# Performance work log

Measured on AMD Instinct MI355X. Metric: run time of the kernel, lower is better.

The kernel has to match this reference:

```python
import jax, jax.numpy as jnp
import numpy as np
from jax import lax

EPS = 1e-5
NBIT = 127.0  # 8-bit symmetric: 2^(8-1)-1

def ste_round(x):
    return x + lax.stop_gradient(jnp.round(x) - x)

def quant_act(x, rng_max):
    # symmetric fake-quant of activations with learned per-cluster range
    s = rng_max / NBIT
    xq = jnp.clip(ste_round(x / s), -NBIT, NBIT) * s
    return xq, s

def fold_bn(w, gamma, beta, mean, var):
    std = jnp.sqrt(var + EPS)
    scale = gamma / std
    w_f = w * scale[:, None, None, None]
    b_f = beta - mean * scale
    return w_f, b_f

def quant_weight(w):
    # per-output-channel symmetric quant
    s = jnp.max(jnp.abs(w), axis=(1, 2, 3), keepdims=True) / NBIT
    wq = jnp.clip(ste_round(w / s), -NBIT, NBIT) * s
    return wq, s.reshape(-1)

def conv(x, w, stride=1, groups=1, pad=0):
    return lax.conv_general_dilated(
        x, w, window_strides=(stride, stride),
        padding=((pad, pad), (pad, pad)),
        dimension_numbers=('NCHW', 'OIHW', 'NCHW'),
        feature_group_count=groups)

def setup_inputs() -> dict:
    key = jax.random.key(0)
    ks = jax.random.split(key, 24)
    B, Cin, H, W = 64, 96, 28, 28
    Cmid, Cout, NC = 576, 96, 4
    d = {}
    d['x'] = jax.random.normal(ks[0], (B, Cin, H, W), dtype=jnp.float32)
    # conv1: 1x1 expansion
    d['w1'] = jax.random.normal(ks[1], (Cmid, Cin, 1, 1), jnp.float32) * 0.1
    d['g1'] = jax.random.uniform(ks[2], (Cmid,), minval=0.5, maxval=1.5)
    d['b1'] = jax.random.normal(ks[3], (Cmid,)) * 0.1
    d['m1'] = jax.random.normal(ks[4], (Cmid,)) * 0.1
    d['v1'] = jax.random.uniform(ks[5], (Cmid,), minval=0.5, maxval=1.5)
    # conv2: 3x3 depthwise
    d['w2'] = jax.random.normal(ks[6], (Cmid, 1, 3, 3), jnp.float32) * 0.1
    d['g2'] = jax.random.uniform(ks[7], (Cmid,), minval=0.5, maxval=1.5)
    d['b2'] = jax.random.normal(ks[8], (Cmid,)) * 0.1
    d['m2'] = jax.random.normal(ks[9], (Cmid,)) * 0.1
    d['v2'] = jax.random.uniform(ks[10], (Cmid,), minval=0.5, maxval=1.5)
    # conv3: 1x1 projection
    d['w3'] = jax.random.normal(ks[11], (Cout, Cmid, 1, 1), jnp.float32) * 0.1
    d['g3'] = jax.random.uniform(ks[12], (Cout,), minval=0.5, maxval=1.5)
    d['b3'] = jax.random.normal(ks[13], (Cout,)) * 0.1
    d['m3'] = jax.random.normal(ks[14], (Cout,)) * 0.1
    d['v3'] = jax.random.uniform(ks[15], (Cout,), minval=0.5, maxval=1.5)
    # per-cluster learned activation ranges for the 4 QuantAct modules
    d['r0'] = jax.random.uniform(ks[16], (NC,), minval=2.0, maxval=8.0)
    d['r1'] = jax.random.uniform(ks[17], (NC,), minval=2.0, maxval=8.0)
    d['r2'] = jax.random.uniform(ks[18], (NC,), minval=2.0, maxval=8.0)
    d['r3'] = jax.random.uniform(ks[19], (NC,), minval=2.0, maxval=8.0)
    d['cluster'] = 2
    return d

def reference(x, w1, g1, b1, m1, v1, w2, g2, b2, m2, v2,
              w3, g3, b3, m3, v3, r0, r1, r2, r3, cluster):
    identity = x  # residual path (in==out, stride==1)
    # QuantAct -> conv1 (BN-folded, per-channel quant) -> ReLU6
    xq, s0 = quant_act(x, r0[cluster])
    w1f, bf1 = fold_bn(w1, g1, b1, m1, v1)
    w1q, ws1 = quant_weight(w1f)
    y = conv(xq, w1q) + bf1[None, :, None, None]
    y = jnp.clip(y, 0.0, 6.0)
    # QuantAct1 -> depthwise conv2 -> ReLU6
    yq, s1 = quant_act(y, r1[cluster])
    w2f, bf2 = fold_bn(w2, g2, b2, m2, v2)
    w2q, ws2 = quant_weight(w2f)
    y = conv(yq, w2q, stride=1, groups=w2.shape[0], pad=1) + bf2[None, :, None, None]
    y = jnp.clip(y, 0.0, 6.0)
    # QuantAct2 -> conv3 projection
    yq, s2 = quant_act(y, r2[cluster])
    w3f, bf3 = fold_bn(w3, g3, b3, m3, v3)
    w3q, ws3 = quant_weight(w3f)
    y = conv(yq, w3q) + bf3[None, :, None, None]
    # residual add, then int32 requant
    y = y + identity
    out, s3 = quant_act(y, r3[cluster])
    return out, s3
```

## Files before the change

kernel.cpp:

```cpp
#include <hip/hip_runtime.h>
#include <cstdint>
#include <cstddef>

typedef int   v4i __attribute__((ext_vector_type(4)));
typedef float v4f __attribute__((ext_vector_type(4)));
typedef unsigned int u32;

constexpr int B_   = 64;
constexpr int CIN  = 96;
constexpr int P_   = 784;
constexpr int CMID = 576;
constexpr int COUT = 96;
constexpr int NOUT = B_ * COUT * P_;
constexpr float NBITF = 127.0f;
constexpr float EPSF  = 1e-5f;


__device__ __forceinline__ int dot3(u32 win, u32 wpk, int acc) {
#if __has_builtin(__builtin_amdgcn_sdot4)
    return __builtin_amdgcn_sdot4((int)win, (int)wpk, acc, false);
#else
    return acc + (int)(signed char)(win)        * (int)(signed char)(wpk)
               + (int)(signed char)(win >> 8)   * (int)(signed char)(wpk >> 8)
               + (int)(signed char)(win >> 16)  * (int)(signed char)(wpk >> 16);
#endif
}

__global__ __launch_bounds__(64)
void prep_weights(const float* __restrict__ w1, const float* __restrict__ g1,
                  const float* __restrict__ b1, const float* __restrict__ m1,
                  const float* __restrict__ v1,
                  const float* __restrict__ w2, const float* __restrict__ g2,
                  const float* __restrict__ b2, const float* __restrict__ m2,
                  const float* __restrict__ v2,
                  const float* __restrict__ w3, const float* __restrict__ g3,
                  const float* __restrict__ b3, const float* __restrict__ m3,
                  const float* __restrict__ v3,
                  int8_t* __restrict__ w1qp, float* __restrict__ ws1, float* __restrict__ bf1,
                  int8_t* __restrict__ w2qi, float* __restrict__ ws2, float* __restrict__ bf2,
                  int8_t* __restrict__ w3qp, float* __restrict__ ws3, float* __restrict__ bf3)
{
    int blk  = blockIdx.x;
    int lane = threadIdx.x;

    const float *w, *g, *bb, *mm, *vv;
    int oc, K, which;
    if (blk < CMID)            { which = 0; w = w1; g = g1; bb = b1; mm = m1; vv = v1; oc = blk;            K = CIN;  }
    else if (blk < 2 * CMID)   { which = 1; w = w2; g = g2; bb = b2; mm = m2; vv = v2; oc = blk - CMID;     K = 9;    }
    else                       { which = 2; w = w3; g = g3; bb = b3; mm = m3; vv = v3; oc = blk - 2 * CMID; K = CMID; }

    float scale = g[oc] / sqrtf(vv[oc] + EPSF);

    float mx = 0.f;
    for (int k = lane; k < K; k += 64)
        mx = fmaxf(mx, fabsf(w[oc * K + k] * scale));
    #pragma unroll
    for (int off = 1; off < 64; off <<= 1)
        mx = fmaxf(mx, __shfl_xor(mx, off));

    float s = mx / NBITF;

    for (int k = lane; k < K; k += 64) {
        float wf = w[oc * K + k] * scale;
        float q  = fminf(fmaxf(rintf(wf / s), -127.f), 127.f);
        if (which == 0)      w1qp[oc * 144 + k] = (int8_t)q;
        else if (which == 1) w2qi[oc * 12 + k]  = (int8_t)q;
        else                 w3qp[oc * 592 + k] = (int8_t)q;
    }
    if (which == 0 && lane < 12)
        ((u32*)(w1qp + oc * 144))[24 + lane] = 0u;
    if (lane == 0) {
        float bf = bb[oc] - mm[oc] * scale;
        if (which == 0)      { ws1[oc] = s; bf1[oc] = bf; }
        else if (which == 1) { ws2[oc] = s; bf2[oc] = bf; }
        else                 { ws3[oc] = s; bf3[oc] = bf; }
    }
}

__global__ __launch_bounds__(256)
void quant_x(const float* __restrict__ x, const float* __restrict__ r0,
             const int* __restrict__ cluster, int8_t* __restrict__ x8t)
{
    __shared__ u32 T[112 * 37];

    int tid = threadIdx.x, pt = blockIdx.x, b = blockIdx.y;
    float inv_s0 = NBITF / r0[cluster[0]];

    for (int i = tid; i < 112 * 13; i += 256) {
        int row = i / 13, cpad = i - row * 13;
        T[row * 37 + 24 + cpad] = 0u;
    }
    for (int u = tid; u < 24 * 28; u += 256) {
        int pq = u % 28, icq = u / 28;
        int pxb = pt * 112 + pq * 4;
        int q[4][4];
        #pragma unroll
        for (int j = 0; j < 4; j++) {
            v4f xv = *(const v4f*)(x + ((size_t)b * CIN + icq * 4 + j) * P_ + pxb);
            #pragma unroll
            for (int i = 0; i < 4; i++)
                q[j][i] = (int)fminf(fmaxf(rintf(xv[i] * inv_s0), -127.f), 127.f);
        }
        #pragma unroll
        for (int i = 0; i < 4; i++) {
            u32 t0 = __builtin_amdgcn_perm((u32)q[1][i], (u32)q[0][i], 0x00000400u);
            u32 t1 = __builtin_amdgcn_perm((u32)q[3][i], (u32)q[2][i], 0x00000400u);
            T[(pq * 4 + i) * 37 + icq] = __builtin_amdgcn_perm(t1, t0, 0x05040100u);
        }
    }
    __syncthreads();
    u32* gdst = (u32*)x8t;
    for (int i = tid; i < 112 * 36; i += 256) {
        int row = i / 36, cc = i - row * 36;
        gdst[((size_t)b * P_ + pt * 112 + row) * 36 + cc] = T[row * 37 + cc];
    }
}

__global__ __launch_bounds__(256)
void conv12(const int8_t* __restrict__ x8t, const int8_t* __restrict__ w1qp,
            const float* __restrict__ ws1, const float* __restrict__ bf1,
            const int8_t* __restrict__ w2qi, const float* __restrict__ ws2,
            const float* __restrict__ bf2,
            const float* __restrict__ r0, const float* __restrict__ r1,
            const float* __restrict__ r2, const int* __restrict__ cluster,
            int8_t* __restrict__ y2qT)
{
    __shared__ int8_t AY[192 * 144];
    __shared__ int8_t y1s[192 * 132];

    int tid = threadIdx.x;
    int b   = blockIdx.y;
    int mt  = blockIdx.x / 14, rt = blockIdx.x - mt * 14;
    int oc0 = mt * 192;
    int R0  = rt * 2;
    int W0  = (R0 - 1) * 28;

    int   c      = cluster[0];
    float s0     = r0[c] / NBITF;
    float s1     = r1[c] / NBITF;
    float inv_s1 = NBITF / r1[c];
    float inv_s2 = NBITF / r2[c];
    float u1     = fminf(rintf(6.f * inv_s1), 127.f);
    float u2     = fminf(rintf(6.f * inv_s2), 127.f);

    {
        const v4i* gsrc = (const v4i*)(w1qp + (size_t)oc0 * 144);
        v4i* ldst = (v4i*)AY;
        for (int i = tid; i < 192 * 9; i += 256) ldst[i] = gsrc[i];
    }
    __syncthreads();

    int lane = tid & 63, wv = tid >> 6;
    int n = lane & 15, q4 = lane >> 4;

    const v4i* bp[7];
    #pragma unroll
    for (int j = 0; j < 7; j++) {
        int px = W0 + j * 16 + n;
        px = min(max(px, 0), P_ - 1);
        bp[j] = (const v4i*)(x8t + ((size_t)b * P_ + px) * 144) + q4;
    }

    v4i acc[3][7];
    #pragma unroll
    for (int i = 0; i < 3; i++)
        #pragma unroll
        for (int j = 0; j < 7; j++) acc[i][j] = (v4i){0, 0, 0, 0};

    const v4i* Af = (const v4i*)AY;
    #pragma unroll
    for (int ks = 0; ks < 2; ks++) {
        v4i bfr[7], afr[3];
        #pragma unroll
        for (int j = 0; j < 7; j++) bfr[j] = bp[j][ks * 4];
        #pragma unroll
        for (int i = 0; i < 3; i++)
            afr[i] = Af[(wv * 48 + i * 16 + n) * 9 + ks * 4 + q4];
        #pragma unroll
        for (int i = 0; i < 3; i++)
            #pragma unroll
            for (int j = 0; j < 7; j++)
                acc[i][j] = __builtin_amdgcn_mfma_i32_16x16x64_i8(afr[i], bfr[j], acc[i][j], 0, 0, 0);
    }

    float sA[3][4], bA[3][4];
    #pragma unroll
    for (int i = 0; i < 3; i++)
        #pragma unroll
        for (int r = 0; r < 4; r++) {
            int oc = oc0 + wv * 48 + i * 16 + q4 * 4 + r;
            sA[i][r] = s0 * ws1[oc] * inv_s1;
            bA[i][r] = bf1[oc] * inv_s1;
        }
    for (int i = tid; i < 192 * 4; i += 256) {
        int ch = i >> 2, r = i & 3;
        int8_t* p = y1s + ch * 132 + r * 32;
        p[0] = 0; p[29] = 0; *(short*)(p + 30) = 0;
    }
    #pragma unroll
    for (int i = 0; i < 3; i++)
        #pragma unroll
        for (int j = 0; j < 7; j++) {
            int pxl = j * 16 + n;
            bool valid = (unsigned)(W0 + pxl) < (unsigned)P_;
            int rowl = pxl / 28, col = pxl - rowl * 28;
            int chl = wv * 48 + i * 16 + q4 * 4;
            #pragma unroll
            for (int r = 0; r < 4; r++) {
                float t = fmaf((float)acc[i][j][r], sA[i][r], bA[i][r]);
                t = fminf(fmaxf(rintf(t), 0.f), u1);
                int lvl = valid ? (int)t : 0;
                y1s[(chl + r) * 132 + rowl * 32 + 1 + col] = (int8_t)lvl;
            }
        }
    __syncthreads();

    int8_t* y2s = AY;
    for (int idx = tid; idx < 192 * 14; idx += 256) {
        int xq   = idx % 7;
        int t2   = idx / 7;
        int orow = t2 & 1;
        int chl  = t2 >> 1;
        int chg  = oc0 + chl;

        const u32* wd = (const u32*)(w2qi + chg * 12);
        u32 wr0 = wd[0], wr1 = wd[1], wr2 = wd[2];
        u32 pk0 = wr0 & 0x00ffffffu;
        u32 pk1 = __builtin_amdgcn_perm(wr1, wr0, 0x00050403u) & 0x00ffffffu;
        u32 pk2 = __builtin_amdgcn_perm(wr2, wr1, 0x00040302u) & 0x00ffffffu;

        const int8_t* base = y1s + chl * 132 + orow * 32;
        int a0 = 0, a1 = 0, a2 = 0, a3 = 0;
        #pragma unroll
        for (int dr = 0; dr < 3; dr++) {
            const u32* row = (const u32*)(base + dr * 32);
            u32 d0 = row[xq], d1 = row[xq + 1];
            u32 pk = (dr == 0) ? pk0 : (dr == 1) ? pk1 : pk2;
            a0 = dot3(d0, pk, a0);
            a1 = dot3(__builtin_amdgcn_alignbyte(d1, d0, 1), pk, a1);
            a2 = dot3(__builtin_amdgcn_alignbyte(d1, d0, 2), pk, a2);
            a3 = dot3(__builtin_amdgcn_alignbyte(d1, d0, 3), pk, a3);
        }
        float sc = s1 * ws2[chg] * inv_s2;
        float bb = bf2[chg] * inv_s2;
        int pxo = orow * 28 + xq * 4;
        int aa[4] = {a0, a1, a2, a3};
        #pragma unroll
        for (int i = 0; i < 4; i++) {
            float t = fmaf((float)aa[i], sc, bb);
            t = fminf(fmaxf(rintf(t), 0.f), u2);
            y2s[(pxo + i) * 200 + chl] = (int8_t)(int)t;
        }
    }
    __syncthreads();

    for (int i = tid; i < 56 * 48; i += 256) {
        int px = i / 48, cq = i - px * 48;
        u32 v = ((const u32*)(y2s + px * 200))[cq];
        ((u32*)y2qT)[((size_t)b * P_ + R0 * 28 + px) * 148 + (oc0 >> 2) + cq] = v;
    }
}

__global__ __launch_bounds__(256)
void conv3_kernel(const int8_t* __restrict__ y2qT, const int8_t* __restrict__ w3qp,
                  const float* __restrict__ ws3, const float* __restrict__ bf3,
                  const float* __restrict__ x, const float* __restrict__ r2,
                  const float* __restrict__ r3, const int* __restrict__ cluster,
                  float* __restrict__ out)
{
    __shared__ int8_t Ash[96 * 592];

    int tid = threadIdx.x, b = blockIdx.y;
    int p0 = blockIdx.x * 64;

    int   c      = cluster[0];
    float s2     = r2[c] / NBITF;
    float s3     = r3[c] / NBITF;
    float inv_s3 = NBITF / r3[c];

    {
        const v4i* gs = (const v4i*)w3qp;
        v4i* ld = (v4i*)Ash;
        for (int i = tid; i < 96 * 37; i += 256) ld[i] = gs[i];
    }
    __syncthreads();

    int lane = tid & 63, wv = tid >> 6;
    int n = lane & 15, q4 = lane >> 4;
    int px  = p0 + wv * 16 + n;
    int pxc = min(px, P_ - 1);

    const v4i* brow = (const v4i*)(y2qT + ((size_t)b * P_ + pxc) * 592) + q4;
    const v4i* Af   = (const v4i*)Ash;

    v4i acc[6];
    #pragma unroll
    for (int i = 0; i < 6; i++) acc[i] = (v4i){0, 0, 0, 0};

    #pragma unroll
    for (int ks = 0; ks < 9; ks++) {
        v4i bfr = brow[ks * 4];
        #pragma unroll
        for (int i = 0; i < 6; i++) {
            v4i afr = Af[(i * 16 + n) * 37 + ks * 4 + q4];
            acc[i] = __builtin_amdgcn_mfma_i32_16x16x64_i8(afr, bfr, acc[i], 0, 0, 0);
        }
    }

    if (px < P_) {
        #pragma unroll
        for (int i = 0; i < 6; i++)
            #pragma unroll
            for (int r = 0; r < 4; r++) {
                int oc = i * 16 + q4 * 4 + r;
                size_t gi = ((size_t)b * COUT + oc) * P_ + px;
                float v  = (float)acc[i][r] * (s2 * ws3[oc]) + bf3[oc] + x[gi];
                float qv = fminf(fmaxf(rintf(v * inv_s3), -127.f), 127.f);
                out[gi] = qv * s3;
            }
    }
    if (blockIdx.x == 0 && blockIdx.y == 0 && tid == 0)
        out[NOUT] = s3;
}

extern "C" void kernel_launch(void* const* d_in, const int* in_sizes, int n_in,
                              void* d_out, int out_size, void* d_ws, size_t ws_size,
                              hipStream_t stream)
{
    const float* x  = (const float*)d_in[0];
    const float* w1 = (const float*)d_in[1];
    const float* g1 = (const float*)d_in[2];
    const float* b1 = (const float*)d_in[3];
    const float* m1 = (const float*)d_in[4];
    const float* v1 = (const float*)d_in[5];
    const float* w2 = (const float*)d_in[6];
    const float* g2 = (const float*)d_in[7];
    const float* b2 = (const float*)d_in[8];
    const float* m2 = (const float*)d_in[9];
    const float* v2 = (const float*)d_in[10];
    const float* w3 = (const float*)d_in[11];
    const float* g3 = (const float*)d_in[12];
    const float* b3 = (const float*)d_in[13];
    const float* m3 = (const float*)d_in[14];
    const float* v3 = (const float*)d_in[15];
    const float* r0 = (const float*)d_in[16];
    const float* r1 = (const float*)d_in[17];
    const float* r2 = (const float*)d_in[18];
    const float* r3 = (const float*)d_in[19];
    const int*   cl = (const int*)d_in[20];

    float* out = (float*)d_out;

    char*  ws  = (char*)d_ws;
    size_t off = 0;
    auto carve = [&](size_t bytes) {
        size_t cur = off;
        off = (off + bytes + 255) & ~(size_t)255;
        return (void*)(ws + cur);
    };
    int8_t* w1qp = (int8_t*)carve((size_t)CMID * 144);
    float*  ws1  = (float*)carve(CMID * 4);
    float*  bf1  = (float*)carve(CMID * 4);
    int8_t* w2qi = (int8_t*)carve((size_t)CMID * 12);
    float*  ws2  = (float*)carve(CMID * 4);
    float*  bf2  = (float*)carve(CMID * 4);
    int8_t* w3qp = (int8_t*)carve((size_t)COUT * 592);
    float*  ws3  = (float*)carve(COUT * 4);
    float*  bf3  = (float*)carve(COUT * 4);
    int8_t* x8t  = (int8_t*)carve((size_t)B_ * P_ * 144);
    int8_t* y2qT = (int8_t*)carve((size_t)B_ * P_ * 592);
    (void)ws_size; (void)in_sizes; (void)n_in; (void)out_size;

    prep_weights<<<dim3(2 * CMID + COUT), dim3(64), 0, stream>>>(
        w1, g1, b1, m1, v1, w2, g2, b2, m2, v2, w3, g3, b3, m3, v3,
        w1qp, ws1, bf1, w2qi, ws2, bf2, w3qp, ws3, bf3);

    quant_x<<<dim3(7, B_), dim3(256), 0, stream>>>(x, r0, cl, x8t);

    conv12<<<dim3(42, B_), dim3(256), 0, stream>>>(
        x8t, w1qp, ws1, bf1, w2qi, ws2, bf2, r0, r1, r2, cl, y2qT);

    conv3_kernel<<<dim3(13, B_), dim3(256), 0, stream>>>(
        y2qT, w3qp, ws3, bf3, x, r2, r3, cl, out);
}
```

Before: 192.3 us.

## Retile int8 intermediates into K-major 64-pixel blocks with packed register transposes

Changes the global layout of the quantized input and the depthwise output from pixel-major rows (144/592 bytes per pixel) to 64-pixel tiles where each 4-channel dword group is contiguous across pixels. MFMA B-fragment loads in conv12 and conv3 become four coalesced dword loads instead of one strided 16-byte load per lane. The shared-memory staging between the 1x1 and depthwise stages is rewritten to pack four channels per dword and transpose with byte-permute instructions instead of doing scattered byte stores. Depthwise weights are also prepacked into 16-byte vectors. The cost is more load instructions per fragment and extra permute work.

```diff
diff --git a/kernel.cpp b/kernel.cpp
--- a/kernel.cpp
+++ b/kernel.cpp
@@ -15,15 +15,30 @@
 constexpr float NBITF = 127.0f;
 constexpr float EPSF  = 1e-5f;
 
-
-__device__ __forceinline__ int dot3(u32 win, u32 wpk, int acc) {
+constexpr int XKD = 36;
+constexpr int YKD = 144;
+constexpr int XBD = 13 * XKD * 64;
+constexpr int YBD = 13 * YKD * 64;
+
+__device__ __forceinline__ int dot3(u32 a, u32 w, int acc) {
 #if __has_builtin(__builtin_amdgcn_sdot4)
-    return __builtin_amdgcn_sdot4((int)win, (int)wpk, acc, false);
+    return __builtin_amdgcn_sdot4((int)a, (int)w, acc, false);
 #else
-    return acc + (int)(signed char)(win)        * (int)(signed char)(wpk)
-               + (int)(signed char)(win >> 8)   * (int)(signed char)(wpk >> 8)
-               + (int)(signed char)(win >> 16)  * (int)(signed char)(wpk >> 16);
+    return acc + (int)(signed char)(a)        * (int)(signed char)(w)
+               + (int)(signed char)(a >> 8)   * (int)(signed char)(w >> 8)
+               + (int)(signed char)(a >> 16)  * (int)(signed char)(w >> 16);
 #endif
+}
+
+__device__ __forceinline__ void tr4(u32 S0, u32 S1, u32 S2, u32 S3, u32 O[4]) {
+    u32 u01 = __builtin_amdgcn_perm(S1, S0, 0x05010400u);
+    u32 u23 = __builtin_amdgcn_perm(S3, S2, 0x05010400u);
+    u32 v01 = __builtin_amdgcn_perm(S1, S0, 0x07030602u);
+    u32 v23 = __builtin_amdgcn_perm(S3, S2, 0x07030602u);
+    O[0] = __builtin_amdgcn_perm(u23, u01, 0x05040100u);
+    O[1] = __builtin_amdgcn_perm(u23, u01, 0x07060302u);
+    O[2] = __builtin_amdgcn_perm(v23, v01, 0x05040100u);
+    O[3] = __builtin_amdgcn_perm(v23, v01, 0x07060302u);
 }
 
 __global__ __launch_bounds__(64)
@@ -37,7 +52,7 @@
                   const float* __restrict__ b3, const float* __restrict__ m3,
                   const float* __restrict__ v3,
                   int8_t* __restrict__ w1qp, float* __restrict__ ws1, float* __restrict__ bf1,
-                  int8_t* __restrict__ w2qi, float* __restrict__ ws2, float* __restrict__ bf2,
+                  v4i* __restrict__ w2pk, float* __restrict__ ws2, float* __restrict__ bf2,
                   int8_t* __restrict__ w3qp, float* __restrict__ ws3, float* __restrict__ bf3)
 {
     int blk  = blockIdx.x;
@@ -60,15 +75,29 @@
 
     float s = mx / NBITF;
 
+    int myq = 0;
     for (int k = lane; k < K; k += 64) {
         float wf = w[oc * K + k] * scale;
         float q  = fminf(fmaxf(rintf(wf / s), -127.f), 127.f);
         if (which == 0)      w1qp[oc * 144 + k] = (int8_t)q;
-        else if (which == 1) w2qi[oc * 12 + k]  = (int8_t)q;
+        else if (which == 1) myq = (int)q;
         else                 w3qp[oc * 592 + k] = (int8_t)q;
     }
     if (which == 0 && lane < 12)
         ((u32*)(w1qp + oc * 144))[24 + lane] = 0u;
+    if (which == 1) {
+        u32 qq[9];
+        #pragma unroll
+        for (int t = 0; t < 9; t++) qq[t] = (u32)__shfl(myq, t, 64) & 0xffu;
+        if (lane == 0) {
+            v4i pk;
+            pk[0] = (int)(qq[0] | (qq[1] << 8) | (qq[2] << 16));
+            pk[1] = (int)(qq[3] | (qq[4] << 8) | (qq[5] << 16));
+            pk[2] = (int)(qq[6] | (qq[7] << 8) | (qq[8] << 16));
+            pk[3] = 0;
+            w2pk[oc] = pk;
+        }
+    }
     if (lane == 0) {
         float bf = bb[oc] - mm[oc] * scale;
         if (which == 0)      { ws1[oc] = s; bf1[oc] = bf; }
@@ -79,20 +108,20 @@
 
 __global__ __launch_bounds__(256)
 void quant_x(const float* __restrict__ x, const float* __restrict__ r0,
-             const int* __restrict__ cluster, int8_t* __restrict__ x8t)
+             const int* __restrict__ cluster, u32* __restrict__ x8t)
 {
     __shared__ u32 T[112 * 37];
 
-    int tid = threadIdx.x, pt = blockIdx.x, b = blockIdx.y;
+    int tid = threadIdx.x, pt0 = blockIdx.x, b = blockIdx.y;
     float inv_s0 = NBITF / r0[cluster[0]];
 
-    for (int i = tid; i < 112 * 13; i += 256) {
-        int row = i / 13, cpad = i - row * 13;
+    for (int i = tid; i < 112 * 12; i += 256) {
+        int row = i / 12, cpad = i - row * 12;
         T[row * 37 + 24 + cpad] = 0u;
     }
     for (int u = tid; u < 24 * 28; u += 256) {
         int pq = u % 28, icq = u / 28;
-        int pxb = pt * 112 + pq * 4;
+        int pxb = pt0 * 112 + pq * 4;
         int q[4][4];
         #pragma unroll
         for (int j = 0; j < 4; j++) {
@@ -109,24 +138,25 @@
         }
     }
     __syncthreads();
-    u32* gdst = (u32*)x8t;
-    for (int i = tid; i < 112 * 36; i += 256) {
-        int row = i / 36, cc = i - row * 36;
-        gdst[((size_t)b * P_ + pt * 112 + row) * 36 + cc] = T[row * 37 + cc];
+    u32* gb = x8t + (size_t)b * XBD;
+    for (int i = tid; i < XKD * 112; i += 256) {
+        int icq = i / 112, pxo = i - icq * 112;
+        int px = pt0 * 112 + pxo;
+        gb[(((px >> 6) * XKD) + icq) * 64 + (px & 63)] = T[pxo * 37 + icq];
     }
 }
 
 __global__ __launch_bounds__(256)
-void conv12(const int8_t* __restrict__ x8t, const int8_t* __restrict__ w1qp,
+void conv12(const u32* __restrict__ x8t, const int8_t* __restrict__ w1qp,
             const float* __restrict__ ws1, const float* __restrict__ bf1,
-            const int8_t* __restrict__ w2qi, const float* __restrict__ ws2,
+            const v4i* __restrict__ w2pk, const float* __restrict__ ws2,
             const float* __restrict__ bf2,
             const float* __restrict__ r0, const float* __restrict__ r1,
             const float* __restrict__ r2, const int* __restrict__ cluster,
-            int8_t* __restrict__ y2qT)
+            u32* __restrict__ y2qT)
 {
-    __shared__ int8_t AY[192 * 144];
-    __shared__ int8_t y1s[192 * 132];
+    __shared__ u32 AY[6912];
+    __shared__ u32 PB[5488];
 
     int tid = threadIdx.x;
     int b   = blockIdx.y;
@@ -144,21 +174,22 @@
     float u2     = fminf(rintf(6.f * inv_s2), 127.f);
 
     {
-        const v4i* gsrc = (const v4i*)(w1qp + (size_t)oc0 * 144);
-        v4i* ldst = (v4i*)AY;
-        for (int i = tid; i < 192 * 9; i += 256) ldst[i] = gsrc[i];
+        const v4i* gs = (const v4i*)(w1qp + (size_t)oc0 * 144);
+        v4i* ld = (v4i*)AY;
+        for (int i = tid; i < 192 * 9; i += 256) ld[i] = gs[i];
     }
     __syncthreads();
 
     int lane = tid & 63, wv = tid >> 6;
     int n = lane & 15, q4 = lane >> 4;
 
-    const v4i* bp[7];
+    const u32* xb = x8t + (size_t)b * XBD;
+    int pbase[7];
     #pragma unroll
     for (int j = 0; j < 7; j++) {
         int px = W0 + j * 16 + n;
         px = min(max(px, 0), P_ - 1);
-        bp[j] = (const v4i*)(x8t + ((size_t)b * P_ + px) * 144) + q4;
+        pbase[j] = ((px >> 6) * XKD) * 64 + (px & 63);
     }
 
     v4i acc[3][7];
@@ -170,9 +201,16 @@
     const v4i* Af = (const v4i*)AY;
     #pragma unroll
     for (int ks = 0; ks < 2; ks++) {
+        int k0 = ks * 16 + q4 * 4;
         v4i bfr[7], afr[3];
         #pragma unroll
-        for (int j = 0; j < 7; j++) bfr[j] = bp[j][ks * 4];
+        for (int j = 0; j < 7; j++) {
+            u32 d0 = xb[pbase[j] + (k0 + 0) * 64];
+            u32 d1 = xb[pbase[j] + (k0 + 1) * 64];
+            u32 d2 = xb[pbase[j] + (k0 + 2) * 64];
+            u32 d3 = xb[pbase[j] + (k0 + 3) * 64];
+            bfr[j] = (v4i){(int)d0, (int)d1, (int)d2, (int)d3};
+        }
         #pragma unroll
         for (int i = 0; i < 3; i++)
             afr[i] = Af[(wv * 48 + i * 16 + n) * 9 + ks * 4 + q4];
@@ -192,50 +230,56 @@
             sA[i][r] = s0 * ws1[oc] * inv_s1;
             bA[i][r] = bf1[oc] * inv_s1;
         }
-    for (int i = tid; i < 192 * 4; i += 256) {
-        int ch = i >> 2, r = i & 3;
-        int8_t* p = y1s + ch * 132 + r * 32;
-        p[0] = 0; p[29] = 0; *(short*)(p + 30) = 0;
-    }
-    #pragma unroll
-    for (int i = 0; i < 3; i++)
+    #pragma unroll
+    for (int i = 0; i < 3; i++) {
+        int chq = wv * 12 + i * 4 + q4;
         #pragma unroll
         for (int j = 0; j < 7; j++) {
             int pxl = j * 16 + n;
             bool valid = (unsigned)(W0 + pxl) < (unsigned)P_;
-            int rowl = pxl / 28, col = pxl - rowl * 28;
-            int chl = wv * 48 + i * 16 + q4 * 4;
+            u32 pk = 0;
             #pragma unroll
             for (int r = 0; r < 4; r++) {
                 float t = fmaf((float)acc[i][j][r], sA[i][r], bA[i][r]);
                 t = fminf(fmaxf(rintf(t), 0.f), u1);
-                int lvl = valid ? (int)t : 0;
-                y1s[(chl + r) * 132 + rowl * 32 + 1 + col] = (int8_t)lvl;
+                pk |= ((u32)(int)t) << (8 * r);
             }
-        }
-    __syncthreads();
-
-    int8_t* y2s = AY;
-    for (int idx = tid; idx < 192 * 14; idx += 256) {
-        int xq   = idx % 7;
-        int t2   = idx / 7;
+            PB[pxl * 49 + chq] = valid ? pk : 0u;
+        }
+    }
+    __syncthreads();
+
+    for (int u = tid; u < 1536; u += 256) {
+        int cc = u & 7, rowl = (u >> 3) & 3, chq = u >> 5;
+        u32 S[4];
+        #pragma unroll
+        for (int k = 0; k < 4; k++) {
+            int col = 4 * cc - 1 + k;
+            S[k] = ((unsigned)col < 28u) ? PB[(rowl * 28 + col) * 49 + chq] : 0u;
+        }
+        u32 O[4];
+        tr4(S[0], S[1], S[2], S[3], O);
+        int bse = chq * 132 + rowl * 8 + cc;
+        #pragma unroll
+        for (int r = 0; r < 4; r++) AY[bse + r * 33] = O[r];
+    }
+    __syncthreads();
+
+    for (int u = tid; u < 2688; u += 256) {
+        int xq = u % 7;
+        int t2 = u / 7;
         int orow = t2 & 1;
         int chl  = t2 >> 1;
         int chg  = oc0 + chl;
 
-        const u32* wd = (const u32*)(w2qi + chg * 12);
-        u32 wr0 = wd[0], wr1 = wd[1], wr2 = wd[2];
-        u32 pk0 = wr0 & 0x00ffffffu;
-        u32 pk1 = __builtin_amdgcn_perm(wr1, wr0, 0x00050403u) & 0x00ffffffu;
-        u32 pk2 = __builtin_amdgcn_perm(wr2, wr1, 0x00040302u) & 0x00ffffffu;
-
-        const int8_t* base = y1s + chl * 132 + orow * 32;
+        v4i wpk = w2pk[chg];
+        int base = chl * 33 + orow * 8;
         int a0 = 0, a1 = 0, a2 = 0, a3 = 0;
         #pragma unroll
         for (int dr = 0; dr < 3; dr++) {
-            const u32* row = (const u32*)(base + dr * 32);
-            u32 d0 = row[xq], d1 = row[xq + 1];
-            u32 pk = (dr == 0) ? pk0 : (dr == 1) ? pk1 : pk2;
+            u32 d0 = AY[base + dr * 8 + xq];
+            u32 d1 = AY[base + dr * 8 + xq + 1];
+            u32 pk = (u32)((dr == 0) ? wpk[0] : (dr == 1) ? wpk[1] : wpk[2]);
             a0 = dot3(d0, pk, a0);
             a1 = dot3(__builtin_amdgcn_alignbyte(d1, d0, 1), pk, a1);
             a2 = dot3(__builtin_amdgcn_alignbyte(d1, d0, 2), pk, a2);
@@ -243,35 +287,46 @@
         }
         float sc = s1 * ws2[chg] * inv_s2;
         float bb = bf2[chg] * inv_s2;
-        int pxo = orow * 28 + xq * 4;
         int aa[4] = {a0, a1, a2, a3};
+        u32 pk2 = 0;
         #pragma unroll
         for (int i = 0; i < 4; i++) {
             float t = fmaf((float)aa[i], sc, bb);
             t = fminf(fmaxf(rintf(t), 0.f), u2);
-            y2s[(pxo + i) * 200 + chl] = (int8_t)(int)t;
-        }
-    }
-    __syncthreads();
-
-    for (int i = tid; i < 56 * 48; i += 256) {
-        int px = i / 48, cq = i - px * 48;
-        u32 v = ((const u32*)(y2s + px * 200))[cq];
-        ((u32*)y2qT)[((size_t)b * P_ + R0 * 28 + px) * 148 + (oc0 >> 2) + cq] = v;
+            pk2 |= ((u32)(int)t) << (8 * i);
+        }
+        PB[chl * 15 + orow * 7 + xq] = pk2;
+    }
+    __syncthreads();
+
+    u32* yb = y2qT + (size_t)b * YBD;
+    int kdw0 = mt * 48;
+    for (int u = tid; u < 672; u += 256) {
+        int pxq = u % 14, chq = u / 14;
+        int orow = pxq / 7, xq = pxq - orow * 7;
+        u32 S[4];
+        #pragma unroll
+        for (int r = 0; r < 4; r++) S[r] = PB[(chq * 4 + r) * 15 + pxq];
+        u32 O[4];
+        tr4(S[0], S[1], S[2], S[3], O);
+        #pragma unroll
+        for (int k = 0; k < 4; k++) {
+            int gpx = (R0 + orow) * 28 + xq * 4 + k;
+            yb[((gpx >> 6) * YKD + kdw0 + chq) * 64 + (gpx & 63)] = O[k];
+        }
     }
 }
 
 __global__ __launch_bounds__(256)
-void conv3_kernel(const int8_t* __restrict__ y2qT, const int8_t* __restrict__ w3qp,
+void conv3_kernel(const u32* __restrict__ y2qT, const int8_t* __restrict__ w3qp,
                   const float* __restrict__ ws3, const float* __restrict__ bf3,
                   const float* __restrict__ x, const float* __restrict__ r2,
                   const float* __restrict__ r3, const int* __restrict__ cluster,
                   float* __restrict__ out)
 {
-    __shared__ int8_t Ash[96 * 592];
-
-    int tid = threadIdx.x, b = blockIdx.y;
-    int p0 = blockIdx.x * 64;
+    __shared__ u32 Ash[96 * 148];
+
+    int tid = threadIdx.x, b = blockIdx.y, pt = blockIdx.x;
 
     int   c      = cluster[0];
     float s2     = r2[c] / NBITF;
@@ -287,11 +342,10 @@
 
     int lane = tid & 63, wv = tid >> 6;
     int n = lane & 15, q4 = lane >> 4;
-    int px  = p0 + wv * 16 + n;
-    int pxc = min(px, P_ - 1);
-
-    const v4i* brow = (const v4i*)(y2qT + ((size_t)b * P_ + pxc) * 592) + q4;
-    const v4i* Af   = (const v4i*)Ash;
+    int pxl = wv * 16 + n;
+
+    const u32* yb = y2qT + (size_t)b * YBD + (size_t)pt * (YKD * 64) + pxl;
+    const v4i* Af = (const v4i*)Ash;
 
     v4i acc[6];
     #pragma unroll
@@ -299,7 +353,12 @@
 
     #pragma unroll
     for (int ks = 0; ks < 9; ks++) {
-        v4i bfr = brow[ks * 4];
+        int k0 = ks * 16 + q4 * 4;
+        u32 d0 = yb[(k0 + 0) * 64];
+        u32 d1 = yb[(k0 + 1) * 64];
+        u32 d2 = yb[(k0 + 2) * 64];
+        u32 d3 = yb[(k0 + 3) * 64];
+        v4i bfr = (v4i){(int)d0, (int)d1, (int)d2, (int)d3};
         #pragma unroll
         for (int i = 0; i < 6; i++) {
             v4i afr = Af[(i * 16 + n) * 37 + ks * 4 + q4];
@@ -307,6 +366,7 @@
         }
     }
 
+    int px = pt * 64 + pxl;
     if (px < P_) {
         #pragma unroll
         for (int i = 0; i < 6; i++)
@@ -319,7 +379,7 @@
                 out[gi] = qv * s3;
             }
     }
-    if (blockIdx.x == 0 && blockIdx.y == 0 && tid == 0)
+    if (pt == 0 && b == 0 && tid == 0)
         out[NOUT] = s3;
 }
 
@@ -361,24 +421,24 @@
     int8_t* w1qp = (int8_t*)carve((size_t)CMID * 144);
     float*  ws1  = (float*)carve(CMID * 4);
     float*  bf1  = (float*)carve(CMID * 4);
-    int8_t* w2qi = (int8_t*)carve((size_t)CMID * 12);
+    v4i*    w2pk = (v4i*)carve((size_t)CMID * 16);
     float*  ws2  = (float*)carve(CMID * 4);
     float*  bf2  = (float*)carve(CMID * 4);
     int8_t* w3qp = (int8_t*)carve((size_t)COUT * 592);
     float*  ws3  = (float*)carve(COUT * 4);
     float*  bf3  = (float*)carve(COUT * 4);
-    int8_t* x8t  = (int8_t*)carve((size_t)B_ * P_ * 144);
-    int8_t* y2qT = (int8_t*)carve((size_t)B_ * P_ * 592);
+    u32*    x8t  = (u32*)carve((size_t)B_ * XBD * 4);
+    u32*    y2qT = (u32*)carve((size_t)B_ * YBD * 4);
     (void)ws_size; (void)in_sizes; (void)n_in; (void)out_size;
 
     prep_weights<<<dim3(2 * CMID + COUT), dim3(64), 0, stream>>>(
         w1, g1, b1, m1, v1, w2, g2, b2, m2, v2, w3, g3, b3, m3, v3,
-        w1qp, ws1, bf1, w2qi, ws2, bf2, w3qp, ws3, bf3);
+        w1qp, ws1, bf1, w2pk, ws2, bf2, w3qp, ws3, bf3);
 
     quant_x<<<dim3(7, B_), dim3(256), 0, stream>>>(x, r0, cl, x8t);
 
     conv12<<<dim3(42, B_), dim3(256), 0, stream>>>(
-        x8t, w1qp, ws1, bf1, w2qi, ws2, bf2, r0, r1, r2, cl, y2qT);
+        x8t, w1qp, ws1, bf1, w2pk, ws2, bf2, r0, r1, r2, cl, y2qT);
 
     conv3_kernel<<<dim3(13, B_), dim3(256), 0, stream>>>(
         y2qT, w3qp, ws3, bf3, x, r2, r3, cl, out);
```

After: 191.0 us. About the same (-0.7%).
